# Optimization experiments

Measured on AMD Instinct MI355X. Metric: run time of the kernel, lower is better.

The kernel has to match this reference:

```python
import jax, jax.numpy as jnp
import numpy as np

BN_EPS = 1e-5


def conv_bn_relu(x, w, b, gamma, beta):
    # Conv2d(stride=2, padding=1) -> BatchNorm2d (training-mode batch stats) -> ReLU
    y = jax.lax.conv_general_dilated(
        x, w, window_strides=(2, 2), padding=((1, 1), (1, 1)),
        dimension_numbers=('NCHW', 'OIHW', 'NCHW')) + b[None, :, None, None]
    mu = y.mean(axis=(0, 2, 3))
    var = y.var(axis=(0, 2, 3))
    y = (y - mu[None, :, None, None]) * jax.lax.rsqrt(var + BN_EPS)[None, :, None, None]
    y = y * gamma[None, :, None, None] + beta[None, :, None, None]
    return jax.nn.relu(y)


def setup_inputs() -> dict:
    key = jax.random.key(0)
    ks = jax.random.split(key, 12)
    N, C, HW_IN = 32, 3, 64
    SD = 24           # stem_dim
    RQ = 128          # rnn_hidden_dim
    MD = 128          # module_dim
    FC = 1024         # classifier hidden
    NA = 2            # num answers
    D_PAIR = (SD + 2) * 2 + RQ  # 180
    s = 0.05
    return {
        'image':   jax.random.normal(ks[0], (N, C, HW_IN, HW_IN), jnp.float32),
        'ques':    jax.random.normal(ks[1], (N, RQ), jnp.float32),
        'conv1_w': jax.random.normal(ks[2], (SD, C, 3, 3), jnp.float32) * s,
        'conv1_b': jnp.zeros((SD,), jnp.float32),
        'bn1_g':   jnp.ones((SD,), jnp.float32),
        'bn1_b':   jnp.zeros((SD,), jnp.float32),
        'conv2_w': jax.random.normal(ks[3], (SD, SD, 3, 3), jnp.float32) * s,
        'conv2_b': jnp.zeros((SD,), jnp.float32),
        'bn2_g':   jnp.ones((SD,), jnp.float32),
        'bn2_b':   jnp.zeros((SD,), jnp.float32),
        'w_rel':   jax.random.normal(ks[4], (D_PAIR, MD), jnp.float32) * s,
        'b_rel':   jnp.zeros((MD,), jnp.float32),
        'w_fc1':   jax.random.normal(ks[5], (MD, FC), jnp.float32) * s,
        'b_fc1':   jnp.zeros((FC,), jnp.float32),
        'w_fc2':   jax.random.normal(ks[6], (FC, NA), jnp.float32) * s,
        'b_fc2':   jnp.zeros((NA,), jnp.float32),
    }


def reference(image, ques, conv1_w, conv1_b, bn1_g, bn1_b,
              conv2_w, conv2_b, bn2_g, bn2_b,
              w_rel, b_rel, w_fc1, b_fc1, w_fc2, b_fc2):
    f = conv_bn_relu(image, conv1_w, conv1_b, bn1_g, bn1_b)
    f = conv_bn_relu(f, conv2_w, conv2_b, bn2_g, bn2_b)
    N, F, H, W = f.shape
    HW = H * W
    flat = f.reshape(N, F, HW).transpose(0, 2, 1)      # (N, HW, F)

    # coordinate grid exactly as in the torch code (stacked over (W, H))
    xs = jnp.linspace(-1.0, 1.0, W)
    ys = jnp.linspace(-1.0, 1.0, H)
    xv = jnp.repeat(xs[:, None], H, axis=1)            # (W, H)
    yv = jnp.repeat(ys[None, :], W, axis=0)            # (W, H)
    coords = jnp.stack([xv, yv], axis=2).reshape(-1, 2)  # (HW, 2)

    fc = jnp.concatenate(
        [flat, jnp.broadcast_to(coords[None], (N, HW, 2))], axis=2)  # (N, HW, F+2)
    D = F + 2

    # relation layer is a single Linear over cat([x_i, x_j, ques]) followed by
    # a sum over ALL (HW)^2 pairs. Because the layer is linear, the pair sum
    # decomposes exactly:
    #   sum_{a,b} (fc[b] Wi + fc[a] Wj + q Wq + b_rel)
    # = HW * (sum_p fc[p]) (Wi + Wj) + HW^2 * (q Wq + b_rel)
    Wi, Wj, Wq = w_rel[:D], w_rel[D:2 * D], w_rel[2 * D:]
    s = fc.sum(axis=1)                                  # (N, D)
    hw = jnp.asarray(HW, fc.dtype)
    relations = hw * (s @ (Wi + Wj)) + (hw * hw) * (ques @ Wq + b_rel)  # (N, 128)

    # ---- classifier: Linear -> ReLU -> Linear ----
    h = jax.nn.relu(relations @ w_fc1 + b_fc1)
    out = h @ w_fc2 + b_fc2                             # (N, num_answers)
    return out
```

## Files before the change

### kernel.cpp

```cpp
#include <hip/hip_runtime.h>
#include <math.h>


#define N_BATCH 32
#define C_OUT 24
#define NBLK 192
#define MAGIC 0x13579BDFu
#define AGENT __HIP_MEMORY_SCOPE_AGENT
#define PITCH 40
#define NROWS 33
#define CHSZ (PITCH * NROWS)

__device__ __forceinline__ float aload(const float* p) {
  return __hip_atomic_load(p, __ATOMIC_RELAXED, AGENT);
}
__device__ __forceinline__ void astore(float* p, float v) {
  __hip_atomic_store(p, v, __ATOMIC_RELAXED, AGENT);
}
__device__ __forceinline__ void waitflag(const unsigned* f) {
  while (__hip_atomic_load(f, __ATOMIC_RELAXED, AGENT) != MAGIC)
    __builtin_amdgcn_s_sleep(1);
}

__global__ __launch_bounds__(1024) void fused_kernel(
    const float* __restrict__ img, const float* __restrict__ ques,
    const float* __restrict__ c1w, const float* __restrict__ c1b,
    const float* __restrict__ g1,  const float* __restrict__ bt1,
    const float* __restrict__ c2w, const float* __restrict__ c2b,
    const float* __restrict__ g2,  const float* __restrict__ bt2,
    const float* __restrict__ w_rel, const float* __restrict__ b_rel,
    const float* __restrict__ w_fc1, const float* __restrict__ b_fc1,
    const float* __restrict__ w_fc2, const float* __restrict__ b_fc2,
    float* __restrict__ out,
    unsigned* __restrict__ flags1, unsigned* __restrict__ flags2,
    unsigned* __restrict__ flags3, unsigned* __restrict__ flags4,
    float* __restrict__ p1, float* __restrict__ p2,
    float* __restrict__ ssum, float* __restrict__ pairs) {
  const int t = threadIdx.x;
  const int bid = blockIdx.x;
  const int lane = t & 63, wid = t >> 6;
  const int n = bid & 31;
  const int r = bid >> 5;

  const int g0 = r * 43 - (r == 5 ? 1 : 0);
  const int gcnt = (r < 4) ? 43 : 42;

  __shared__ unsigned short y1u[24 * CHSZ];
  __align__(16) __shared__ float red[5120];
  __shared__ float s_a[C_OUT], s_b[C_OUT];
  __shared__ float a2[4], b2[4];
  __shared__ float chS[16], chS2[16];
  __shared__ float qpart[1024];
  __shared__ float qfull[128];
  __shared__ float s_s[26];
  __shared__ float s_coef[128];

  if (t < 24 * PITCH) {
    int ch = t / PITCH;
    y1u[ch * CHSZ + (t - ch * PITCH)] = 0;
  }
  if (t < 768)
    y1u[(t >> 5) * CHSZ + ((t & 31) + 1) * PITCH] = 0;

  {
    int oh = t >> 5, ow = t & 31;
    float win[27];
    #pragma unroll
    for (int ci = 0; ci < 3; ci++)
      #pragma unroll
      for (int kh = 0; kh < 3; kh++) {
        int ih = oh * 2 - 1 + kh;
        #pragma unroll
        for (int kw = 0; kw < 3; kw++) {
          int iw = ow * 2 - 1 + kw;
          win[ci * 9 + kh * 3 + kw] =
              (ih >= 0 && iw >= 0) ? img[(n * 3 + ci) * 4096 + ih * 64 + iw] : 0.f;
        }
      }
    #pragma unroll
    for (int co = 0; co < C_OUT; co++) {
      float acc = c1b[co];
      #pragma unroll
      for (int q = 0; q < 27; q++) acc += win[q] * c1w[co * 27 + q];
      unsigned bits = __float_as_uint(acc);
      unsigned rr = (bits + 0x7FFFu + ((bits >> 16) & 1u)) >> 16;
      y1u[co * CHSZ + (oh + 1) * PITCH + (ow + 1)] = (unsigned short)rr;
    }
  }
  __syncthreads();

  if (r == 0) {
    if (t < 768) {
      int ch = t >> 5, l = t & 31;
      float s = 0.f, s2 = 0.f;
      #pragma unroll
      for (int i = 0; i < 32; i++) {
        float x = __uint_as_float(
            (unsigned)y1u[ch * CHSZ + (i + 1) * PITCH + (l + 1)] << 16);
        s += x; s2 += x * x;
      }
      #pragma unroll
      for (int off = 16; off > 0; off >>= 1) {
        s += __shfl_down(s, off, 32);
        s2 += __shfl_down(s2, off, 32);
      }
      if (l == 0) {
        astore(&p1[ch * 32 + n], s);
        astore(&p1[768 + ch * 32 + n], s2);
      }
    }
    __syncthreads();
    if (t == 0)
      __hip_atomic_store(&flags1[n], MAGIC, __ATOMIC_RELEASE, AGENT);
  }

  {
    float pf = 0.f;
    {
      int row = t >> 3, l = t & 7;
      int col = g0 * 4 + l * 32;
      col = col < 1024 ? col : 1023;
      pf += w_fc1[row * 1024 + col];
    }
    if (t < 720) pf += w_rel[t * 32];
    if (t < 64)  pf += w_fc2[t * 32];
    if (t < 32)  pf += b_fc1[t * 32];
    asm volatile("" :: "v"(pf));
  }

  if (t < 32) waitflag(&flags1[t]);
  __syncthreads();
  if (t < 768) {
    int ch = t >> 5, j = t & 31;
    float s = aload(&p1[ch * 32 + j]);
    float s2 = aload(&p1[768 + ch * 32 + j]);
    #pragma unroll
    for (int off = 16; off > 0; off >>= 1) {
      s += __shfl_down(s, off, 32);
      s2 += __shfl_down(s2, off, 32);
    }
    if (j == 0) {
      float mu = s * (1.f / 32768.f);
      float var = s2 * (1.f / 32768.f) - mu * mu;
      float a = rsqrtf(var + 1e-5f) * g1[ch];
      s_a[ch] = a;
      s_b[ch] = bt1[ch] - mu * a;
    }
  }
  __syncthreads();

  const int px = t & 255;
  const int slot = t >> 8;
  const int co2 = r * 4 + slot;
  float acc2;
  {
    const int o2h = px >> 4, o2w = px & 15;
    float accq[4] = {0.f, 0.f, 0.f, 0.f};
    const int ci0 = slot * 6;
    #pragma unroll
    for (int cc = 0; cc < 6; cc++) {
      const int ci = ci0 + cc;
      const float a1 = s_a[ci], b1 = s_b[ci];
      const unsigned* chp = (const unsigned*)(y1u + ci * CHSZ);
      #pragma unroll
      for (int kh = 0; kh < 3; kh++) {
        const int row = o2h * 2 + kh;
        const unsigned* pr = chp + row * (PITCH / 2);
        unsigned w0 = pr[o2w];
        unsigned w1 = pr[o2w + 1];
        float x0 = __uint_as_float(w0 << 16);
        float x1 = __uint_as_float(w0 & 0xffff0000u);
        float x2 = __uint_as_float(w1 << 16);
        x0 = fmaxf(fmaf(x0, a1, b1), 0.f);
        x1 = fmaxf(fmaf(x1, a1, b1), 0.f);
        x2 = fmaxf(fmaf(x2, a1, b1), 0.f);
        if (row == 0) { x0 = 0.f; x1 = 0.f; x2 = 0.f; }
        if (o2w == 0) x0 = 0.f;
        #pragma unroll
        for (int co = 0; co < 4; co++) {
          const float* wp = c2w + ((r * 4 + co) * C_OUT + ci) * 9 + kh * 3;
          accq[co] = fmaf(x0, wp[0], accq[co]);
          accq[co] = fmaf(x1, wp[1], accq[co]);
          accq[co] = fmaf(x2, wp[2], accq[co]);
        }
      }
    }
    #pragma unroll
    for (int q = 0; q < 4; q++) red[(slot * 256 + px) * 5 + q] = accq[q];
  }
  __syncthreads();
  {
    acc2 = c2b[co2];
    #pragma unroll
    for (int s = 0; s < 4; s++) acc2 += red[(s * 256 + px) * 5 + slot];
  }
  {
    float s = acc2, s2 = acc2 * acc2;
    #pragma unroll
    for (int off = 32; off > 0; off >>= 1) {
      s += __shfl_down(s, off, 64);
      s2 += __shfl_down(s2, off, 64);
    }
    if (lane == 0) { chS[slot * 4 + (wid & 3)] = s; chS2[slot * 4 + (wid & 3)] = s2; }
  }
  __syncthreads();
  if (t < 4) {
    float s = chS[t * 4] + chS[t * 4 + 1] + chS[t * 4 + 2] + chS[t * 4 + 3];
    float s2 = chS2[t * 4] + chS2[t * 4 + 1] + chS2[t * 4 + 2] + chS2[t * 4 + 3];
    astore(&p2[(r * 4 + t) * 32 + n], s);
    astore(&p2[768 + (r * 4 + t) * 32 + n], s2);
  }
  __syncthreads();
  if (t == 0)
    __hip_atomic_store(&flags2[bid], MAGIC, __ATOMIC_RELEASE, AGENT);

  {
    int m = t & 127, g = t >> 7;
    const float* qv = ques + n * 128;
    float q = 0.f;
    for (int k = g * 16; k < g * 16 + 16; k++)
      q += qv[k] * w_rel[(52 + k) * 128 + m];
    qpart[t] = q;
  }
  __syncthreads();
  if (t < 128) {
    float q = b_rel[t];
    #pragma unroll
    for (int g = 0; g < 8; g++) q += qpart[g * 128 + t];
    qfull[t] = 65536.f * q;
  }

  if (t < 32) waitflag(&flags2[r * 32 + t]);
  __syncthreads();
  if (t < 128) {
    int c4 = t >> 5, j = t & 31;
    float s = aload(&p2[(r * 4 + c4) * 32 + j]);
    float s2 = aload(&p2[768 + (r * 4 + c4) * 32 + j]);
    #pragma unroll
    for (int off = 16; off > 0; off >>= 1) {
      s += __shfl_down(s, off, 32);
      s2 += __shfl_down(s2, off, 32);
    }
    if (j == 0) {
      float mu = s * (1.f / 8192.f);
      float var = s2 * (1.f / 8192.f) - mu * mu;
      float a = rsqrtf(var + 1e-5f) * g2[r * 4 + c4];
      a2[c4] = a;
      b2[c4] = bt2[r * 4 + c4] - mu * a;
    }
  }
  __syncthreads();

  {
    float v = acc2 * a2[slot] + b2[slot];
    v = v > 0.f ? v : 0.f;
    #pragma unroll
    for (int off = 32; off > 0; off >>= 1) v += __shfl_down(v, off, 64);
    if (lane == 0) chS[slot * 4 + (wid & 3)] = v;
  }
  __syncthreads();
  if (t < 4)
    astore(&ssum[n * C_OUT + r * 4 + t],
           chS[t * 4] + chS[t * 4 + 1] + chS[t * 4 + 2] + chS[t * 4 + 3]);
  __syncthreads();
  if (t == 0)
    __hip_atomic_store(&flags3[bid], MAGIC, __ATOMIC_RELEASE, AGENT);

  if (t < 6 && t != r) waitflag(&flags3[t * 32 + n]);
  __syncthreads();
  if (t < C_OUT) s_s[t] = aload(&ssum[n * C_OUT + t]);
  if (t == 24 || t == 25) {
    float cs = 0.f;
    for (int i = 0; i < 16; i++) cs += -1.f + 2.f * (float)i / 15.f;
    s_s[t] = 16.f * cs;
  }
  __syncthreads();

  {
    int col = t & 127, g = t >> 7;
    float p = 0.f;
    #pragma unroll
    for (int dd = 0; dd < 4; dd++) {
      int d = g + dd * 8;
      if (d < 26)
        p += s_s[d] * (w_rel[d * 128 + col] + w_rel[(26 + d) * 128 + col]);
    }
    qpart[t] = p;
  }
  __syncthreads();
  if (t < 128) {
    float sterm = 0.f;
    #pragma unroll
    for (int g = 0; g < 8; g++) sterm += qpart[g * 128 + t];
    s_coef[t] = qfull[t] + 256.f * sterm;
  }
  __syncthreads();

  {
    const int gi = lane, mseg = wid;
    if (gi < gcnt) {
      const float4* wp = (const float4*)w_fc1 + (g0 + gi);
      float4 acc = make_float4(0.f, 0.f, 0.f, 0.f);
      #pragma unroll
      for (int k = 0; k < 8; k++) {
        int m = mseg * 8 + k;
        float c = s_coef[m];
        float4 w = wp[m * 256];
        acc.x += c * w.x; acc.y += c * w.y; acc.z += c * w.z; acc.w += c * w.w;
      }
      ((float4*)red)[mseg * 43 + gi] = acc;
    }
  }
  __syncthreads();
  float a0 = 0.f, a1 = 0.f;
  if (t < gcnt * 4) {
    const int gcol = g0 * 4 + t;
    float h = b_fc1[gcol];
    #pragma unroll
    for (int mseg = 0; mseg < 16; mseg++) h += red[mseg * 172 + t];
    h = h > 0.f ? h : 0.f;
    a0 = h * w_fc2[2 * gcol];
    a1 = h * w_fc2[2 * gcol + 1];
  }
  __syncthreads();
  {
    #pragma unroll
    for (int off = 32; off > 0; off >>= 1) {
      a0 += __shfl_down(a0, off, 64);
      a1 += __shfl_down(a1, off, 64);
    }
    if (lane == 0) { chS[wid] = a0; chS2[wid] = a1; }
  }
  __syncthreads();
  if (t == 0) {
    float b0 = 0.f, b1v = 0.f;
    #pragma unroll
    for (int i = 0; i < 16; i++) { b0 += chS[i]; b1v += chS2[i]; }
    if (r != 0) {
      astore(&pairs[n * 12 + r * 2 + 0], b0);
      astore(&pairs[n * 12 + r * 2 + 1], b1v);
      __hip_atomic_store(&flags4[bid], MAGIC, __ATOMIC_RELEASE, AGENT);
    } else {
      chS[0] = b0; chS2[0] = b1v;
    }
  }
  if (r != 0) return;

  if (t >= 1 && t < 6) waitflag(&flags4[t * 32 + n]);
  __syncthreads();
  if (t == 0) {
    float b0 = chS[0], b1v = chS2[0];
    #pragma unroll
    for (int i = 1; i < 6; i++) {
      b0 += aload(&pairs[n * 12 + i * 2 + 0]);
      b1v += aload(&pairs[n * 12 + i * 2 + 1]);
    }
    out[n * 2 + 0] = b0 + b_fc2[0];
    out[n * 2 + 1] = b1v + b_fc2[1];
  }
}

extern "C" void kernel_launch(void* const* d_in, const int* in_sizes, int n_in,
                              void* d_out, int out_size, void* d_ws, size_t ws_size,
                              hipStream_t stream) {
  const float* image   = (const float*)d_in[0];
  const float* ques    = (const float*)d_in[1];
  const float* conv1_w = (const float*)d_in[2];
  const float* conv1_b = (const float*)d_in[3];
  const float* bn1_g   = (const float*)d_in[4];
  const float* bn1_b   = (const float*)d_in[5];
  const float* conv2_w = (const float*)d_in[6];
  const float* conv2_b = (const float*)d_in[7];
  const float* bn2_g   = (const float*)d_in[8];
  const float* bn2_b   = (const float*)d_in[9];
  const float* w_rel   = (const float*)d_in[10];
  const float* b_rel   = (const float*)d_in[11];
  const float* w_fc1   = (const float*)d_in[12];
  const float* b_fc1   = (const float*)d_in[13];
  const float* w_fc2   = (const float*)d_in[14];
  const float* b_fc2   = (const float*)d_in[15];
  float* out = (float*)d_out;

  unsigned* flags1 = (unsigned*)d_ws;
  unsigned* flags2 = flags1 + 32;
  unsigned* flags3 = flags2 + 192;
  unsigned* flags4 = flags3 + 192;
  float* p1    = (float*)d_ws + 608;
  float* p2    = p1 + 1536;
  float* ssum  = p2 + 1536;
  float* pairs = ssum + 768;

  fused_kernel<<<NBLK, 1024, 0, stream>>>(
      image, ques, conv1_w, conv1_b, bn1_g, bn1_b, conv2_w, conv2_b,
      bn2_g, bn2_b, w_rel, b_rel, w_fc1, b_fc1, w_fc2, b_fc2,
      out, flags1, flags2, flags3, flags4, p1, p2, ssum, pairs);
}
```

Baseline: 124.4 us.

## Add 256-block fused kernel splitting output channels across blocks with global conv1 exchange

Adds a new fused kernel that launches 256 blocks (8 channel segments per image) instead of 192. Each block computes conv1 for only 3 output channels and writes them to a global bf16 buffer, then gathers all 24 channels from its peer blocks before computing conv2 for its 3 channels. The classifier FC1 is also split across segments, with segment 0 reducing the partial results. This spreads the conv work over more CUs in exchange for more inter-block flag synchronisation and global traffic, and it falls back to the old kernel if the workspace is too small.

```diff
diff --git a/kernel.cpp b/kernel.cpp
--- a/kernel.cpp
+++ b/kernel.cpp
@@ -2,14 +2,12 @@
 #include <math.h>
 
 
-#define N_BATCH 32
-#define C_OUT 24
-#define NBLK 192
 #define MAGIC 0x13579BDFu
 #define AGENT __HIP_MEMORY_SCOPE_AGENT
 #define PITCH 40
 #define NROWS 33
 #define CHSZ (PITCH * NROWS)
+#define C_OUT 24
 
 __device__ __forceinline__ float aload(const float* p) {
   return __hip_atomic_load(p, __ATOMIC_RELAXED, AGENT);
@@ -17,12 +15,360 @@
 __device__ __forceinline__ void astore(float* p, float v) {
   __hip_atomic_store(p, v, __ATOMIC_RELAXED, AGENT);
 }
+__device__ __forceinline__ unsigned aloadu(const unsigned* p) {
+  return __hip_atomic_load(p, __ATOMIC_RELAXED, AGENT);
+}
+__device__ __forceinline__ void astoreu(unsigned* p, unsigned v) {
+  __hip_atomic_store(p, v, __ATOMIC_RELAXED, AGENT);
+}
 __device__ __forceinline__ void waitflag(const unsigned* f) {
   while (__hip_atomic_load(f, __ATOMIC_RELAXED, AGENT) != MAGIC)
     __builtin_amdgcn_s_sleep(1);
 }
 
-__global__ __launch_bounds__(1024) void fused_kernel(
+__global__ __launch_bounds__(1024) void fused_wide(
+    const float* __restrict__ img, const float* __restrict__ ques,
+    const float* __restrict__ c1w, const float* __restrict__ c1b,
+    const float* __restrict__ g1,  const float* __restrict__ bt1,
+    const float* __restrict__ c2w, const float* __restrict__ c2b,
+    const float* __restrict__ g2,  const float* __restrict__ bt2,
+    const float* __restrict__ w_rel, const float* __restrict__ b_rel,
+    const float* __restrict__ w_fc1, const float* __restrict__ b_fc1,
+    const float* __restrict__ w_fc2, const float* __restrict__ b_fc2,
+    float* __restrict__ out,
+    unsigned* __restrict__ flags1, unsigned* __restrict__ flags2,
+    unsigned* __restrict__ flags3, unsigned* __restrict__ flags4,
+    float* __restrict__ p1, float* __restrict__ p2,
+    float* __restrict__ ssum, float* __restrict__ pairs,
+    unsigned* __restrict__ y1g) {
+  const int t = threadIdx.x;
+  const int bid = blockIdx.x;
+  const int lane = t & 63, wid = t >> 6;
+  const int n = bid & 31;
+  const int seg = bid >> 5;
+  const int cobase = seg * 3;
+
+  __shared__ __align__(16) unsigned short y1u[24 * CHSZ];
+  __align__(16) __shared__ float red[5120];
+  __shared__ float s_a[C_OUT], s_b[C_OUT];
+  __shared__ float a2[3], b2[3];
+  __shared__ float chS[64], chS2[64];
+  __shared__ float qpart[1024];
+  __shared__ float qfull[128];
+  __shared__ float s_s[26];
+  __shared__ float s_coef[128];
+  unsigned* lds32 = (unsigned*)y1u;
+
+  {
+    const int oh = t >> 5, ow = t & 31;
+    float win[27];
+    #pragma unroll
+    for (int ci = 0; ci < 3; ci++)
+      #pragma unroll
+      for (int kh = 0; kh < 3; kh++) {
+        int ih = oh * 2 - 1 + kh;
+        #pragma unroll
+        for (int kw = 0; kw < 3; kw++) {
+          int iw = ow * 2 - 1 + kw;
+          win[ci * 9 + kh * 3 + kw] =
+              (ih >= 0 && iw >= 0) ? img[(n * 3 + ci) * 4096 + ih * 64 + iw] : 0.f;
+        }
+      }
+    unsigned x16[3]; float xb[3];
+    #pragma unroll
+    for (int j = 0; j < 3; j++) {
+      const int co = cobase + j;
+      float acc = c1b[co];
+      #pragma unroll
+      for (int q = 0; q < 27; q++) acc += win[q] * c1w[co * 27 + q];
+      unsigned bits = __float_as_uint(acc);
+      unsigned rr = (bits + 0x7FFFu + ((bits >> 16) & 1u)) >> 16;
+      x16[j] = rr;
+      xb[j] = __uint_as_float(rr << 16);
+    }
+    const unsigned base = ((unsigned)(n * 24 + cobase) * 32 + oh) * 17;
+    #pragma unroll
+    for (int j = 0; j < 3; j++) {
+      unsigned up = (unsigned)__shfl_down((int)x16[j], 1, 64);
+      const unsigned rb = base + (unsigned)j * 544;
+      if (ow & 1) {
+        unsigned hi = (ow == 31) ? 0u : up;
+        astoreu(&y1g[rb + ((unsigned)(ow + 1) >> 1)], x16[j] | (hi << 16));
+      } else if (ow == 0) {
+        astoreu(&y1g[rb], x16[j] << 16);
+      }
+    }
+    #pragma unroll
+    for (int j = 0; j < 3; j++) {
+      float s = xb[j], s2 = xb[j] * xb[j];
+      #pragma unroll
+      for (int off = 32; off > 0; off >>= 1) {
+        s += __shfl_down(s, off, 64);
+        s2 += __shfl_down(s2, off, 64);
+      }
+      if (lane == 0) { chS[j * 16 + wid] = s; chS2[j * 16 + wid] = s2; }
+    }
+  }
+  __syncthreads();
+  if (t < 3) {
+    float s = 0.f, s2 = 0.f;
+    #pragma unroll
+    for (int i = 0; i < 16; i++) { s += chS[t * 16 + i]; s2 += chS2[t * 16 + i]; }
+    astore(&p1[(cobase + t) * 32 + n], s);
+    astore(&p1[768 + (cobase + t) * 32 + n], s2);
+  }
+  __syncthreads();
+  if (t == 0)
+    __hip_atomic_store(&flags1[bid], MAGIC, __ATOMIC_RELEASE, AGENT);
+
+  {
+    float pf = 0.f;
+    if (t < 512) pf += w_fc1[(t >> 2) * 1024 + seg * 128 + (t & 3) * 32];
+    if (t < 720) pf += w_rel[t * 32];
+    if (t < 8)   pf += w_fc2[seg * 256 + t * 32];
+    if (t < 4)   pf += b_fc1[seg * 128 + t * 32];
+    asm volatile("" :: "v"(pf));
+  }
+
+  if (t < 8 && t != seg) waitflag(&flags1[t * 32 + n]);
+  __syncthreads();
+  {
+    const unsigned* yg = y1g + n * 13056;
+    for (int i = t; i < 13056; i += 1024) {
+      unsigned v = aloadu(yg + i);
+      int co = i / 544;
+      int rem = i - co * 544;
+      int row = rem / 17;
+      int c = rem - row * 17;
+      lds32[co * 660 + (row + 1) * 20 + c] = v;
+    }
+  }
+  if (t < 256) waitflag(&flags1[t]);
+  __syncthreads();
+  if (t < 768) {
+    int ch = t >> 5, j = t & 31;
+    float s = aload(&p1[ch * 32 + j]);
+    float s2 = aload(&p1[768 + ch * 32 + j]);
+    #pragma unroll
+    for (int off = 16; off > 0; off >>= 1) {
+      s += __shfl_down(s, off, 32);
+      s2 += __shfl_down(s2, off, 32);
+    }
+    if (j == 0) {
+      float mu = s * (1.f / 32768.f);
+      float var = s2 * (1.f / 32768.f) - mu * mu;
+      float a = rsqrtf(var + 1e-5f) * g1[ch];
+      s_a[ch] = a;
+      s_b[ch] = bt1[ch] - mu * a;
+    }
+  }
+  __syncthreads();
+
+  const int px = t & 255;
+  const int slot = t >> 8;
+  {
+    const int o2h = px >> 4, o2w = px & 15;
+    float accq[3] = {0.f, 0.f, 0.f};
+    const int ci0 = slot * 6;
+    #pragma unroll
+    for (int cc = 0; cc < 6; cc++) {
+      const int ci = ci0 + cc;
+      const float a1 = s_a[ci], b1 = s_b[ci];
+      const unsigned* chp = lds32 + ci * 660;
+      #pragma unroll
+      for (int kh = 0; kh < 3; kh++) {
+        const int row = o2h * 2 + kh;
+        const unsigned* pr = chp + row * 20;
+        unsigned w0 = pr[o2w];
+        unsigned w1 = pr[o2w + 1];
+        float x0 = __uint_as_float(w0 << 16);
+        float x1 = __uint_as_float(w0 & 0xffff0000u);
+        float x2 = __uint_as_float(w1 << 16);
+        x0 = fmaxf(fmaf(x0, a1, b1), 0.f);
+        x1 = fmaxf(fmaf(x1, a1, b1), 0.f);
+        x2 = fmaxf(fmaf(x2, a1, b1), 0.f);
+        if (row == 0) { x0 = 0.f; x1 = 0.f; x2 = 0.f; }
+        if (o2w == 0) x0 = 0.f;
+        #pragma unroll
+        for (int j = 0; j < 3; j++) {
+          const float* wp = c2w + ((cobase + j) * C_OUT + ci) * 9 + kh * 3;
+          accq[j] = fmaf(x0, wp[0], fmaf(x1, wp[1], fmaf(x2, wp[2], accq[j])));
+        }
+      }
+    }
+    #pragma unroll
+    for (int j = 0; j < 3; j++) red[(slot * 256 + px) * 5 + j] = accq[j];
+  }
+  __syncthreads();
+  float acc2 = 0.f;
+  const int j2 = t >> 8;
+  if (t < 768) {
+    acc2 = c2b[cobase + j2];
+    #pragma unroll
+    for (int s = 0; s < 4; s++) acc2 += red[(s * 256 + px) * 5 + j2];
+    float s = acc2, s2 = acc2 * acc2;
+    #pragma unroll
+    for (int off = 32; off > 0; off >>= 1) {
+      s += __shfl_down(s, off, 64);
+      s2 += __shfl_down(s2, off, 64);
+    }
+    if (lane == 0) { chS[j2 * 4 + (wid & 3)] = s; chS2[j2 * 4 + (wid & 3)] = s2; }
+  }
+  __syncthreads();
+  if (t < 3) {
+    float s = chS[t * 4] + chS[t * 4 + 1] + chS[t * 4 + 2] + chS[t * 4 + 3];
+    float s2 = chS2[t * 4] + chS2[t * 4 + 1] + chS2[t * 4 + 2] + chS2[t * 4 + 3];
+    astore(&p2[(cobase + t) * 32 + n], s);
+    astore(&p2[768 + (cobase + t) * 32 + n], s2);
+  }
+  __syncthreads();
+  if (t == 0)
+    __hip_atomic_store(&flags2[bid], MAGIC, __ATOMIC_RELEASE, AGENT);
+
+  {
+    int m = t & 127, g = t >> 7;
+    const float* qv = ques + n * 128;
+    float q = 0.f;
+    for (int k = g * 16; k < g * 16 + 16; k++)
+      q += qv[k] * w_rel[(52 + k) * 128 + m];
+    qpart[t] = q;
+  }
+  __syncthreads();
+  if (t < 128) {
+    float q = b_rel[t];
+    #pragma unroll
+    for (int g = 0; g < 8; g++) q += qpart[g * 128 + t];
+    qfull[t] = 65536.f * q;
+  }
+
+  if (t < 256) waitflag(&flags2[t]);
+  __syncthreads();
+  if (t < 96) {
+    int j = t >> 5, l = t & 31;
+    float s = aload(&p2[(cobase + j) * 32 + l]);
+    float s2 = aload(&p2[768 + (cobase + j) * 32 + l]);
+    #pragma unroll
+    for (int off = 16; off > 0; off >>= 1) {
+      s += __shfl_down(s, off, 32);
+      s2 += __shfl_down(s2, off, 32);
+    }
+    if (l == 0) {
+      float mu = s * (1.f / 8192.f);
+      float var = s2 * (1.f / 8192.f) - mu * mu;
+      float a = rsqrtf(var + 1e-5f) * g2[cobase + j];
+      a2[j] = a;
+      b2[j] = bt2[cobase + j] - mu * a;
+    }
+  }
+  __syncthreads();
+
+  if (t < 768) {
+    float v = acc2 * a2[j2] + b2[j2];
+    v = v > 0.f ? v : 0.f;
+    #pragma unroll
+    for (int off = 32; off > 0; off >>= 1) v += __shfl_down(v, off, 64);
+    if (lane == 0) chS[j2 * 4 + (wid & 3)] = v;
+  }
+  __syncthreads();
+  if (t < 3)
+    astore(&ssum[n * C_OUT + cobase + t],
+           chS[t * 4] + chS[t * 4 + 1] + chS[t * 4 + 2] + chS[t * 4 + 3]);
+  __syncthreads();
+  if (t == 0)
+    __hip_atomic_store(&flags3[bid], MAGIC, __ATOMIC_RELEASE, AGENT);
+
+  if (t < 8 && t != seg) waitflag(&flags3[t * 32 + n]);
+  __syncthreads();
+  if (t < C_OUT) s_s[t] = aload(&ssum[n * C_OUT + t]);
+  if (t == 24 || t == 25) {
+    float cs = 0.f;
+    for (int i = 0; i < 16; i++) cs += -1.f + 2.f * (float)i / 15.f;
+    s_s[t] = 16.f * cs;
+  }
+  __syncthreads();
+  {
+    int col = t & 127, g = t >> 7;
+    float p = 0.f;
+    #pragma unroll
+    for (int dd = 0; dd < 4; dd++) {
+      int d = g + dd * 8;
+      if (d < 26)
+        p += s_s[d] * (w_rel[d * 128 + col] + w_rel[(26 + d) * 128 + col]);
+    }
+    qpart[t] = p;
+  }
+  __syncthreads();
+  if (t < 128) {
+    float sterm = 0.f;
+    #pragma unroll
+    for (int g = 0; g < 8; g++) sterm += qpart[g * 128 + t];
+    s_coef[t] = qfull[t] + 256.f * sterm;
+  }
+  __syncthreads();
+
+  {
+    const int gi = t & 31, ms = t >> 5;
+    const float4* wp = (const float4*)w_fc1 + seg * 32 + gi;
+    float4 a4 = make_float4(0.f, 0.f, 0.f, 0.f);
+    #pragma unroll
+    for (int k = 0; k < 4; k++) {
+      int m = ms * 4 + k;
+      float c = s_coef[m];
+      float4 w = wp[m * 256];
+      a4.x = fmaf(c, w.x, a4.x); a4.y = fmaf(c, w.y, a4.y);
+      a4.z = fmaf(c, w.z, a4.z); a4.w = fmaf(c, w.w, a4.w);
+    }
+    red[(gi * 4 + 0) * 33 + ms] = a4.x;
+    red[(gi * 4 + 1) * 33 + ms] = a4.y;
+    red[(gi * 4 + 2) * 33 + ms] = a4.z;
+    red[(gi * 4 + 3) * 33 + ms] = a4.w;
+  }
+  __syncthreads();
+  float a0 = 0.f, a1v = 0.f;
+  if (t < 128) {
+    float h = b_fc1[seg * 128 + t];
+    #pragma unroll
+    for (int ms = 0; ms < 32; ms++) h += red[t * 33 + ms];
+    h = h > 0.f ? h : 0.f;
+    a0 = h * w_fc2[(seg * 128 + t) * 2];
+    a1v = h * w_fc2[(seg * 128 + t) * 2 + 1];
+  }
+  {
+    #pragma unroll
+    for (int off = 32; off > 0; off >>= 1) {
+      a0 += __shfl_down(a0, off, 64);
+      a1v += __shfl_down(a1v, off, 64);
+    }
+    if (t < 128 && lane == 0) { chS[wid] = a0; chS2[wid] = a1v; }
+  }
+  __syncthreads();
+  if (t == 0) {
+    float b0 = chS[0] + chS[1], b1 = chS2[0] + chS2[1];
+    if (seg != 0) {
+      astore(&pairs[n * 16 + seg * 2 + 0], b0);
+      astore(&pairs[n * 16 + seg * 2 + 1], b1);
+      __hip_atomic_store(&flags4[bid], MAGIC, __ATOMIC_RELEASE, AGENT);
+    } else {
+      s_coef[0] = b0; s_coef[1] = b1;
+    }
+  }
+  if (seg != 0) return;
+
+  if (t >= 1 && t < 8) waitflag(&flags4[t * 32 + n]);
+  __syncthreads();
+  if (t == 0) {
+    float b0 = s_coef[0], b1 = s_coef[1];
+    #pragma unroll
+    for (int i = 1; i < 8; i++) {
+      b0 += aload(&pairs[n * 16 + i * 2 + 0]);
+      b1 += aload(&pairs[n * 16 + i * 2 + 1]);
+    }
+    out[n * 2 + 0] = b0 + b_fc2[0];
+    out[n * 2 + 1] = b1 + b_fc2[1];
+  }
+}
+
+__global__ __launch_bounds__(1024) void fused_kernel_r3(
     const float* __restrict__ img, const float* __restrict__ ques,
     const float* __restrict__ c1w, const float* __restrict__ c1b,
     const float* __restrict__ g1,  const float* __restrict__ bt1,
@@ -41,7 +387,6 @@
   const int lane = t & 63, wid = t >> 6;
   const int n = bid & 31;
   const int r = bid >> 5;
-
   const int g0 = r * 43 - (r == 5 ? 1 : 0);
   const int gcnt = (r < 4) ? 43 : 42;
 
@@ -381,17 +726,33 @@
   const float* b_fc2   = (const float*)d_in[15];
   float* out = (float*)d_out;
 
-  unsigned* flags1 = (unsigned*)d_ws;
-  unsigned* flags2 = flags1 + 32;
-  unsigned* flags3 = flags2 + 192;
-  unsigned* flags4 = flags3 + 192;
-  float* p1    = (float*)d_ws + 608;
-  float* p2    = p1 + 1536;
-  float* ssum  = p2 + 1536;
-  float* pairs = ssum + 768;
-
-  fused_kernel<<<NBLK, 1024, 0, stream>>>(
-      image, ques, conv1_w, conv1_b, bn1_g, bn1_b, conv2_w, conv2_b,
-      bn2_g, bn2_b, w_rel, b_rel, w_fc1, b_fc1, w_fc2, b_fc2,
-      out, flags1, flags2, flags3, flags4, p1, p2, ssum, pairs);
+  const size_t WIDE_WORDS = 1024 + 1536 + 1536 + 768 + 512 + 417792;
+  if (ws_size >= WIDE_WORDS * 4) {
+    unsigned* flags1 = (unsigned*)d_ws;
+    unsigned* flags2 = flags1 + 256;
+    unsigned* flags3 = flags2 + 256;
+    unsigned* flags4 = flags3 + 256;
+    float* p1    = (float*)(flags4 + 256);
+    float* p2    = p1 + 1536;
+    float* ssum  = p2 + 1536;
+    float* pairs = ssum + 768;
+    unsigned* y1g = (unsigned*)(pairs + 512);
+    fused_wide<<<256, 1024, 0, stream>>>(
+        image, ques, conv1_w, conv1_b, bn1_g, bn1_b, conv2_w, conv2_b,
+        bn2_g, bn2_b, w_rel, b_rel, w_fc1, b_fc1, w_fc2, b_fc2,
+        out, flags1, flags2, flags3, flags4, p1, p2, ssum, pairs, y1g);
+  } else {
+    unsigned* flags1 = (unsigned*)d_ws;
+    unsigned* flags2 = flags1 + 32;
+    unsigned* flags3 = flags2 + 192;
+    unsigned* flags4 = flags3 + 192;
+    float* p1    = (float*)d_ws + 608;
+    float* p2    = p1 + 1536;
+    float* ssum  = p2 + 1536;
+    float* pairs = ssum + 768;
+    fused_kernel_r3<<<192, 1024, 0, stream>>>(
+        image, ques, conv1_w, conv1_b, bn1_g, bn1_b, conv2_w, conv2_b,
+        bn2_g, bn2_b, w_rel, b_rel, w_fc1, b_fc1, w_fc2, b_fc2,
+        out, flags1, flags2, flags3, flags4, p1, p2, ssum, pairs);
+  }
 }
```

Measured after the change: 122.4 us. Within noise of the previous version (-1.6%).
